# Optimization experiments

Measured on AMD Instinct MI355X. Metric: run time of the kernel, lower is better.

Reference implementation:

```python
import jax, jax.numpy as jnp
import numpy as np

DN = ('NCHW', 'OIHW', 'NCHW')
BLOB_HW = 16  # hard-coded in make_gaussian_blob_maps

_ENC = [(32, 3), (32, 32), (64, 32), (64, 64), (128, 64), (128, 128), (128, 128)]
_DEC = [(64, 128), (64, 64), (32, 64), (32, 32), (16, 32), (16, 16)]


def _conv(x, w, b, stride):
    y = jax.lax.conv_general_dilated(x, w, (stride, stride), 'SAME', dimension_numbers=DN)
    return y + b[None, :, None, None]


def _tconv(x, w, b):
    # decoder stride-2 stage: 'iteratively doubling the input width'
    y = jax.lax.conv_transpose(x, w, (2, 2), 'SAME', dimension_numbers=DN)
    return y + b[None, :, None, None]


def setup_inputs() -> dict:
    key = jax.random.key(0)
    keys = jax.random.split(key, 1 + 2 * (len(_ENC) + len(_DEC)))
    inp = {'x': jax.random.normal(keys[0], (4, 8, 3, 128, 128), jnp.float32)}
    i = 1
    for j, (o, c) in enumerate(_ENC):
        inp[f'enc_w{j}'] = 0.05 * jax.random.normal(keys[i], (o, c, 3, 3), jnp.float32); i += 1
        inp[f'enc_b{j}'] = 0.05 * jax.random.normal(keys[i], (o,), jnp.float32); i += 1
    for j, (o, c) in enumerate(_DEC):
        inp[f'dec_w{j}'] = 0.05 * jax.random.normal(keys[i], (o, c, 3, 3), jnp.float32); i += 1
        inp[f'dec_b{j}'] = 0.05 * jax.random.normal(keys[i], (o,), jnp.float32); i += 1
    return inp


def _forward(x, enc_w0, enc_b0, enc_w1, enc_b1, enc_w2, enc_b2, enc_w3, enc_b3,
             enc_w4, enc_b4, enc_w5, enc_b5, enc_w6, enc_b6,
             dec_w0, dec_b0, dec_w1, dec_b1, dec_w2, dec_b2,
             dec_w3, dec_b3, dec_w4, dec_b4, dec_w5, dec_b5):
    N, T = x.shape[0], x.shape[1]
    xi = x.reshape((N * T,) + x.shape[2:])  # (B, 3, 128, 128)
    # ---- encoder ----
    h = _conv(xi, enc_w0, enc_b0, 1)                              # Identity act
    h = _conv(h, enc_w1, enc_b1, 1)                               # Identity act
    h = jax.nn.leaky_relu(_conv(h, enc_w2, enc_b2, 2), 0.2)       # 128 -> 64
    h = jax.nn.leaky_relu(_conv(h, enc_w3, enc_b3, 1), 0.2)
    h = jax.nn.leaky_relu(_conv(h, enc_w4, enc_b4, 2), 0.2)       # 64 -> 32
    h = jax.nn.leaky_relu(_conv(h, enc_w5, enc_b5, 1), 0.2)
    R = jax.nn.softplus(_conv(h, enc_w6, enc_b6, 2))              # (B, K, 16, 16)
    B, K, H, W = R.shape
    # ---- keypoint presence: mean over spatial dims ----
    mu = R.sum((2, 3)) / (H * W)                                  # (B, K)
    # ---- normalize_feature_maps: faithful net effect of the in-place loop,
    # which ends up dividing each batch item by the ORIGINAL sum of its LAST map ----
    denom = R[:, K - 1].sum((1, 2))                               # (B,)
    D = R / denom[:, None, None, None]
    # ---- average_feature_maps: spatial-index weighted sum (soft-argmax) ----
    gh = jnp.arange(H, dtype=R.dtype)
    gw = jnp.arange(W, dtype=R.dtype)
    c0 = jnp.einsum('bkhw,h->bk', D, gh)                          # row coord
    c1 = jnp.einsum('bkhw,w->bk', D, gw)                          # col coord
    # ---- gaussian blob maps: mu * exp(-0.5 * ||(u,v) - c||^2), sigma = 1 ----
    u = jnp.arange(BLOB_HW, dtype=R.dtype)[:, None]               # (16, 1)
    v = jnp.arange(BLOB_HW, dtype=R.dtype)[None, :]               # (1, 16)
    d2 = (u[None, None] - c0[:, :, None, None]) ** 2 + (v[None, None] - c1[:, :, None, None]) ** 2
    maps = mu[:, :, None, None] * jnp.exp(-0.5 * d2)              # (B, K, 16, 16)
    # ---- decoder ----
    g = jax.nn.relu(_tconv(maps, dec_w0, dec_b0))                 # 16 -> 32
    g = jax.nn.relu(_conv(g, dec_w1, dec_b1, 1))
    g = jax.nn.relu(_tconv(g, dec_w2, dec_b2))                    # 32 -> 64
    g = jax.nn.relu(_conv(g, dec_w3, dec_b3, 1))
    g = jax.nn.relu(_tconv(g, dec_w4, dec_b4))                    # 64 -> 128
    g = jax.nn.relu(_conv(g, dec_w5, dec_b5, 1))
    return g  # original forward returns the un-reshaped (N*T, C, H, W) tensor


def reference(x, enc_w0, enc_b0, enc_w1, enc_b1, enc_w2, enc_b2, enc_w3, enc_b3,
              enc_w4, enc_b4, enc_w5, enc_b5, enc_w6, enc_b6,
              dec_w0, dec_b0, dec_w1, dec_b1, dec_w2, dec_b2,
              dec_w3, dec_b3, dec_w4, dec_b4, dec_w5, dec_b5):
    return _forward(x, enc_w0, enc_b0, enc_w1, enc_b1, enc_w2, enc_b2, enc_w3, enc_b3,
                    enc_w4, enc_b4, enc_w5, enc_b5, enc_w6, enc_b6,
                    dec_w0, dec_b0, dec_w1, dec_b1, dec_w2, dec_b2,
                    dec_w3, dec_b3, dec_w4, dec_b4, dec_w5, dec_b5)
```

## Files before the change

kernel.cpp:

```cpp
#include <hip/hip_runtime.h>
#include <math.h>


enum { ACT_ID = 0, ACT_LRELU = 1, ACT_SOFTPLUS = 2, ACT_RELU = 3 };

template<int ACT>
__device__ __forceinline__ float act_fn(float x) {
  if (ACT == ACT_LRELU)    return x >= 0.f ? x : 0.2f * x;
  if (ACT == ACT_SOFTPLUS) return fmaxf(x, 0.f) + log1pf(expf(-fabsf(x)));
  if (ACT == ACT_RELU)     return fmaxf(x, 0.f);
  return x;
}

template<int ACT, int NC, int CPT>
__global__ __launch_bounds__(256)
void conv_s1(const float* __restrict__ in, const float* __restrict__ w,
             const float* __restrict__ bias, float* __restrict__ out,
             int Cin, int Cout, int H, int W) {
  const int cogs = Cout / NC;
  const int gx  = blockIdx.x;
  const int cog = gx % cogs;
  const int b   = gx / cogs;
  const int co0 = cog * NC;
  const int Wq  = W / CPT;
  const int items = H * Wq;
  const int item  = blockIdx.y * 256 + threadIdx.x;
  if (item >= items) return;
  const int y  = item / Wq;
  const int x0 = (item - y * Wq) * CPT;

  const int HW = H * W;
  const float* ib = in + (size_t)b * Cin * HW;

  const bool okT = (y > 0), okB = (y < H - 1);
  const bool okL = (x0 > 0), okR = (x0 + CPT < W);
  const int ym = okT ? (y - 1) : 0;
  const int yp = okB ? (y + 1) : 0;
  const int xl = okL ? (x0 - 1) : 0;
  const int xr = okR ? (x0 + CPT) : 0;

  float acc[NC][CPT];
  #pragma unroll
  for (int u = 0; u < NC; ++u)
    #pragma unroll
    for (int q = 0; q < CPT; ++q) acc[u][q] = 0.f;

  for (int ci = 0; ci < Cin; ++ci) {
    const float* p = ib + ci * HW;
    const float* wci = w + ((size_t)co0 * Cin + ci) * 9;
    #pragma unroll
    for (int dy = 0; dy < 3; ++dy) {
      const int  ry    = (dy == 0) ? ym : ((dy == 1) ? y : yp);
      const bool okRow = (dy == 0) ? okT : ((dy == 1) ? true : okB);
      const float* r = p + ry * W;
      float v[CPT + 2];
      if (CPT == 4) {
        float  lf = r[xl];
        float4 m  = *(const float4*)(r + x0);
        float  rf = r[xr];
        v[0] = (okRow && okL) ? lf : 0.f;
        v[1] = okRow ? m.x : 0.f;
        v[2] = okRow ? m.y : 0.f;
        v[3] = okRow ? m.z : 0.f;
        v[4] = okRow ? m.w : 0.f;
        v[5] = (okRow && okR) ? rf : 0.f;
      } else {
        v[0] = (okRow && okL) ? r[xl] : 0.f;
        #pragma unroll
        for (int q = 0; q < CPT; ++q) v[1 + q] = okRow ? r[x0 + q] : 0.f;
        v[CPT + 1] = (okRow && okR) ? r[xr] : 0.f;
      }
      #pragma unroll
      for (int u = 0; u < NC; ++u) {
        const float* wp = wci + (size_t)u * Cin * 9 + dy * 3;
        const float w0 = wp[0], w1 = wp[1], w2 = wp[2];
        #pragma unroll
        for (int q = 0; q < CPT; ++q)
          acc[u][q] += v[q] * w0 + v[q + 1] * w1 + v[q + 2] * w2;
      }
    }
  }

  #pragma unroll
  for (int u = 0; u < NC; ++u) {
    const float bv = bias[co0 + u];
    float* op = out + ((size_t)(b * Cout + co0 + u) * H + y) * W + x0;
    if (CPT == 4) {
      float4 r4;
      r4.x = act_fn<ACT>(acc[u][0] + bv);
      r4.y = act_fn<ACT>(acc[u][1] + bv);
      r4.z = act_fn<ACT>(acc[u][2] + bv);
      r4.w = act_fn<ACT>(acc[u][3] + bv);
      *(float4*)op = r4;
    } else {
      #pragma unroll
      for (int q = 0; q < CPT; ++q) op[q] = act_fn<ACT>(acc[u][q] + bv);
    }
  }
}

template<int ACT, int NC, int CPT>
__global__ __launch_bounds__(256)
void conv_s2(const float* __restrict__ in, const float* __restrict__ w,
             const float* __restrict__ bias, float* __restrict__ out,
             int Cin, int Cout, int H, int W) {
  const int Ho = H >> 1, Wo = W >> 1;
  const int cogs = Cout / NC;
  const int gx  = blockIdx.x;
  const int cog = gx % cogs;
  const int b   = gx / cogs;
  const int co0 = cog * NC;
  const int Wq  = Wo / CPT;
  const int items = Ho * Wq;
  const int item  = blockIdx.y * 256 + threadIdx.x;
  if (item >= items) return;
  const int y  = item / Wq;
  const int x0 = (item - y * Wq) * CPT;
  const int ix = 2 * x0;

  const int HW = H * W;
  const float* ib = in + (size_t)b * Cin * HW;

  const int iy0 = 2 * y, iy1 = 2 * y + 1, iy2 = 2 * y + 2;
  const bool okB = (iy2 < H);
  const int iy2c = okB ? iy2 : 0;
  const bool okR = (ix + 2 * CPT < W);
  const int ixr  = okR ? (ix + 2 * CPT) : 0;

  float acc[NC][CPT];
  #pragma unroll
  for (int u = 0; u < NC; ++u)
    #pragma unroll
    for (int q = 0; q < CPT; ++q) acc[u][q] = 0.f;

  for (int ci = 0; ci < Cin; ++ci) {
    const float* p = ib + ci * HW;
    const float* wci = w + ((size_t)co0 * Cin + ci) * 9;
    #pragma unroll
    for (int dy = 0; dy < 3; ++dy) {
      const int  ry    = (dy == 0) ? iy0 : ((dy == 1) ? iy1 : iy2c);
      const bool okRow = (dy < 2) || okB;
      const float* r = p + ry * W;
      float v[2 * CPT + 1];
      if (CPT == 4) {
        float4 m0 = *(const float4*)(r + ix);
        float4 m1 = *(const float4*)(r + ix + 4);
        float  rf = r[ixr];
        v[0] = okRow ? m0.x : 0.f; v[1] = okRow ? m0.y : 0.f;
        v[2] = okRow ? m0.z : 0.f; v[3] = okRow ? m0.w : 0.f;
        v[4] = okRow ? m1.x : 0.f; v[5] = okRow ? m1.y : 0.f;
        v[6] = okRow ? m1.z : 0.f; v[7] = okRow ? m1.w : 0.f;
        v[8] = (okRow && okR) ? rf : 0.f;
      } else {
        #pragma unroll
        for (int q = 0; q < 2 * CPT; ++q) v[q] = okRow ? r[ix + q] : 0.f;
        v[2 * CPT] = (okRow && okR) ? r[ixr] : 0.f;
      }
      #pragma unroll
      for (int u = 0; u < NC; ++u) {
        const float* wp = wci + (size_t)u * Cin * 9 + dy * 3;
        const float w0 = wp[0], w1 = wp[1], w2 = wp[2];
        #pragma unroll
        for (int q = 0; q < CPT; ++q)
          acc[u][q] += v[2*q] * w0 + v[2*q + 1] * w1 + v[2*q + 2] * w2;
      }
    }
  }

  #pragma unroll
  for (int u = 0; u < NC; ++u) {
    const float bv = bias[co0 + u];
    float* op = out + ((size_t)(b * Cout + co0 + u) * Ho + y) * Wo + x0;
    if (CPT == 4) {
      float4 r4;
      r4.x = act_fn<ACT>(acc[u][0] + bv);
      r4.y = act_fn<ACT>(acc[u][1] + bv);
      r4.z = act_fn<ACT>(acc[u][2] + bv);
      r4.w = act_fn<ACT>(acc[u][3] + bv);
      *(float4*)op = r4;
    } else {
      #pragma unroll
      for (int q = 0; q < CPT; ++q) op[q] = act_fn<ACT>(acc[u][q] + bv);
    }
  }
}

template<int ACT, int NC>
__global__ __launch_bounds__(256)
void tconv(const float* __restrict__ in, const float* __restrict__ w,
           const float* __restrict__ bias, float* __restrict__ out,
           int Cin, int Cout, int Hin) {
  const int cogs = Cout / NC;
  const int gx  = blockIdx.x;
  const int cog = gx % cogs;
  const int b   = gx / cogs;
  const int co0 = cog * NC;
  const int items = Hin * Hin;
  const int item  = blockIdx.y * 256 + threadIdx.x;
  if (item >= items) return;
  const int i = item / Hin;
  const int j = item - i * Hin;

  const float* ib = in + (size_t)b * Cin * items;
  const bool okT = (i > 0), okL = (j > 0);
  const int im = okT ? i - 1 : 0;
  const int jm = okL ? j - 1 : 0;

  float a00[NC], a01[NC], a10[NC], a11[NC];
  #pragma unroll
  for (int u = 0; u < NC; ++u) { a00[u]=0.f; a01[u]=0.f; a10[u]=0.f; a11[u]=0.f; }

  for (int ci = 0; ci < Cin; ++ci) {
    const float* p = ib + ci * items;
    float xtl = p[im*Hin + jm]; xtl = (okT && okL) ? xtl : 0.f;
    float xtr = p[im*Hin + j];  xtr = okT ? xtr : 0.f;
    float xbl = p[i*Hin + jm];  xbl = okL ? xbl : 0.f;
    float xbr = p[i*Hin + j];
    const float* wci = w + ((size_t)co0 * Cin + ci) * 9;
    #pragma unroll
    for (int u = 0; u < NC; ++u) {
      const float* wp = wci + (size_t)u * Cin * 9;
      const float w00 = wp[0], w01 = wp[1], w02 = wp[2];
      const float w10 = wp[3], w11 = wp[4], w12 = wp[5];
      const float w20 = wp[6], w21 = wp[7], w22 = wp[8];
      a00[u] += xtl*w00 + xtr*w02 + xbl*w20 + xbr*w22;
      a01[u] += xtr*w01 + xbr*w21;
      a10[u] += xbl*w10 + xbr*w12;
      a11[u] += xbr*w11;
    }
  }

  const int Ho = Hin * 2;
  #pragma unroll
  for (int u = 0; u < NC; ++u) {
    const float bv = bias[co0 + u];
    float* op = out + (size_t)(b * Cout + co0 + u) * Ho * Ho + (2*i) * Ho + 2*j;
    float2 t0, t1;
    t0.x = act_fn<ACT>(a00[u] + bv); t0.y = act_fn<ACT>(a01[u] + bv);
    t1.x = act_fn<ACT>(a10[u] + bv); t1.y = act_fn<ACT>(a11[u] + bv);
    *(float2*)op = t0;
    *(float2*)(op + Ho) = t1;
  }
}

__global__ __launch_bounds__(64)
void kp_reduce(const float* __restrict__ R, float* __restrict__ S,
               float* __restrict__ Sh, float* __restrict__ Sw) {
  const int bk = blockIdx.x;
  const int t = threadIdx.x;
  const float* p = R + (size_t)bk * 256;
  float s = 0.f, sh = 0.f, sw = 0.f;
  #pragma unroll
  for (int q = 0; q < 4; ++q) {
    int idx = t + q * 64;
    float v = p[idx];
    s  += v;
    sh += v * (float)(idx >> 4);
    sw += v * (float)(idx & 15);
  }
  #pragma unroll
  for (int off = 32; off > 0; off >>= 1) {
    s  += __shfl_down(s, off);
    sh += __shfl_down(sh, off);
    sw += __shfl_down(sw, off);
  }
  if (t == 0) { S[bk] = s; Sh[bk] = sh; Sw[bk] = sw; }
}

__global__ __launch_bounds__(256)
void kp_maps(const float* __restrict__ S, const float* __restrict__ Sh,
             const float* __restrict__ Sw, float* __restrict__ maps, int K) {
  const int bk = blockIdx.x;
  const int b = bk / K;
  const int t = threadIdx.x;
  const float s   = S[bk];
  const float den = S[b * K + (K - 1)];
  const float mu  = s * (1.0f / 256.0f);
  const float c0  = Sh[bk] / den;
  const float c1  = Sw[bk] / den;
  const float u = (float)(t >> 4);
  const float v = (float)(t & 15);
  const float d2 = (u - c0) * (u - c0) + (v - c1) * (v - c1);
  maps[(size_t)bk * 256 + t] = mu * expf(-0.5f * d2);
}

extern "C" void kernel_launch(void* const* d_in, const int* in_sizes, int n_in,
                              void* d_out, int out_size, void* d_ws, size_t ws_size,
                              hipStream_t stream) {
  const int B = 32;
  const float* x = (const float*)d_in[0];
  const float* ew[7]; const float* eb[7];
  for (int j = 0; j < 7; ++j) { ew[j] = (const float*)d_in[1 + 2*j]; eb[j] = (const float*)d_in[2 + 2*j]; }
  const float* dw[6]; const float* db[6];
  for (int j = 0; j < 6; ++j) { dw[j] = (const float*)d_in[15 + 2*j]; db[j] = (const float*)d_in[16 + 2*j]; }

  float* ws   = (float*)d_ws;
  float* bufA = ws;
  float* bufB = bufA + 16777216;
  float* R    = bufB + 16777216;
  float* maps = R + 1048576;
  float* S    = maps + 1048576;
  float* Sh   = S + 4096;
  float* Sw   = Sh + 4096;
  float* outp = (float*)d_out;

  dim3 blk(256);

  conv_s1<ACT_ID,      8,4><<<dim3(B*4,  16), blk, 0, stream>>>(x,    ew[0], eb[0], bufA, 3,   32,  128, 128);
  conv_s1<ACT_ID,      8,4><<<dim3(B*4,  16), blk, 0, stream>>>(bufA, ew[1], eb[1], bufB, 32,  32,  128, 128);
  conv_s2<ACT_LRELU,   8,4><<<dim3(B*8,   4), blk, 0, stream>>>(bufB, ew[2], eb[2], bufA, 32,  64,  128, 128);
  conv_s1<ACT_LRELU,   8,4><<<dim3(B*8,   4), blk, 0, stream>>>(bufA, ew[3], eb[3], bufB, 64,  64,  64,  64);
  conv_s2<ACT_LRELU,   8,4><<<dim3(B*16,  1), blk, 0, stream>>>(bufB, ew[4], eb[4], bufA, 64,  128, 64,  64);
  conv_s1<ACT_LRELU,   8,4><<<dim3(B*16,  1), blk, 0, stream>>>(bufA, ew[5], eb[5], bufB, 128, 128, 32,  32);
  conv_s2<ACT_SOFTPLUS,8,1><<<dim3(B*16,  1), blk, 0, stream>>>(bufB, ew[6], eb[6], R,    128, 128, 32,  32);

  kp_reduce<<<dim3(B*128), dim3(64), 0, stream>>>(R, S, Sh, Sw);
  kp_maps  <<<dim3(B*128), blk, 0, stream>>>(S, Sh, Sw, maps, 128);

  tconv<ACT_RELU,   8>  <<<dim3(B*8,   1), blk, 0, stream>>>(maps, dw[0], db[0], bufA, 128, 64, 16);
  conv_s1<ACT_RELU, 8,4><<<dim3(B*8,   1), blk, 0, stream>>>(bufA, dw[1], db[1], bufB, 64,  64, 32, 32);
  tconv<ACT_RELU,   8>  <<<dim3(B*4,   4), blk, 0, stream>>>(bufB, dw[2], db[2], bufA, 64,  32, 32);
  conv_s1<ACT_RELU, 8,4><<<dim3(B*4,   4), blk, 0, stream>>>(bufA, dw[3], db[3], bufB, 32,  32, 64, 64);
  tconv<ACT_RELU,   8>  <<<dim3(B*2,  16), blk, 0, stream>>>(bufB, dw[4], db[4], bufA, 32,  16, 64);
  conv_s1<ACT_RELU, 8,4><<<dim3(B*2,  16), blk, 0, stream>>>(bufA, dw[5], db[5], outp, 16,  16, 128, 128);
}
```

Measured before the change: 1.375 ms.

## Split-K over input channels for small-spatial convs, double-buffer loads, retune tiles

Adds a split-K template parameter so the low-resolution convolutions divide input channels across two grid slices, writing partial sums that a new combine kernel adds together with bias and activation applied. This raises the block count for layers that previously launched only a few blocks per image. It also software-pipelines the per-channel loads (double-buffered registers) in the conv and tconv kernels, and lowers columns-per-thread or channels-per-block for several layers to expose more threads. In exchange it adds extra partial-sum global traffic and extra kernel launches.

New measurement: 1.320 ms. 4.0% less time.

```diff
diff --git a/kernel.cpp b/kernel.cpp
--- a/kernel.cpp
+++ b/kernel.cpp
@@ -12,11 +12,11 @@
   return x;
 }
 
-template<int ACT, int NC, int CPT>
+template<int ACT, int NC, int CPT, int KS>
 __global__ __launch_bounds__(256)
 void conv_s1(const float* __restrict__ in, const float* __restrict__ w,
              const float* __restrict__ bias, float* __restrict__ out,
-             int Cin, int Cout, int H, int W) {
+             int Cin, int Cout, int H, int W, size_t kstride) {
   const int cogs = Cout / NC;
   const int gx  = blockIdx.x;
   const int cog = gx % cogs;
@@ -31,6 +31,10 @@
 
   const int HW = H * W;
   const float* ib = in + (size_t)b * Cin * HW;
+  const int nci = Cin / KS;
+  const int ci0 = (KS > 1) ? (int)blockIdx.z * nci : 0;
+  const int ci1 = ci0 + nci;
+  float* outbase = out + ((KS > 1) ? (size_t)blockIdx.z * kstride : 0);
 
   const bool okT = (y > 0), okB = (y < H - 1);
   const bool okL = (x0 > 0), okR = (x0 + CPT < W);
@@ -41,69 +45,109 @@
 
   float acc[NC][CPT];
   #pragma unroll
-  for (int u = 0; u < NC; ++u)
+  for (int u = 0; u < NC; ++u) {
     #pragma unroll
     for (int q = 0; q < CPT; ++q) acc[u][q] = 0.f;
-
-  for (int ci = 0; ci < Cin; ++ci) {
+  }
+
+  constexpr int RV = CPT + 2;
+
+  auto load_rows = [&](float* v, int ci) {
     const float* p = ib + ci * HW;
-    const float* wci = w + ((size_t)co0 * Cin + ci) * 9;
     #pragma unroll
     for (int dy = 0; dy < 3; ++dy) {
-      const int  ry    = (dy == 0) ? ym : ((dy == 1) ? y : yp);
+      const int ry = (dy == 0) ? ym : ((dy == 1) ? y : yp);
+      const float* r = p + ry * W;
+      float* o = v + dy * RV;
+      o[0] = r[xl];
+      if constexpr (CPT == 4) {
+        float4 m = *(const float4*)(r + x0);
+        o[1] = m.x; o[2] = m.y; o[3] = m.z; o[4] = m.w;
+      } else if constexpr (CPT == 2) {
+        float2 m = *(const float2*)(r + x0);
+        o[1] = m.x; o[2] = m.y;
+      } else {
+        #pragma unroll
+        for (int q = 0; q < CPT; ++q) o[1 + q] = r[x0 + q];
+      }
+      o[CPT + 1] = r[xr];
+    }
+  };
+
+  auto fma_rows = [&](float* v, int ci) {
+    #pragma unroll
+    for (int dy = 0; dy < 3; ++dy) {
       const bool okRow = (dy == 0) ? okT : ((dy == 1) ? true : okB);
-      const float* r = p + ry * W;
-      float v[CPT + 2];
-      if (CPT == 4) {
-        float  lf = r[xl];
-        float4 m  = *(const float4*)(r + x0);
-        float  rf = r[xr];
-        v[0] = (okRow && okL) ? lf : 0.f;
-        v[1] = okRow ? m.x : 0.f;
-        v[2] = okRow ? m.y : 0.f;
-        v[3] = okRow ? m.z : 0.f;
-        v[4] = okRow ? m.w : 0.f;
-        v[5] = (okRow && okR) ? rf : 0.f;
-      } else {
-        v[0] = (okRow && okL) ? r[xl] : 0.f;
-        #pragma unroll
-        for (int q = 0; q < CPT; ++q) v[1 + q] = okRow ? r[x0 + q] : 0.f;
-        v[CPT + 1] = (okRow && okR) ? r[xr] : 0.f;
-      }
+      float* o = v + dy * RV;
+      o[0] = (okRow && okL) ? o[0] : 0.f;
       #pragma unroll
-      for (int u = 0; u < NC; ++u) {
-        const float* wp = wci + (size_t)u * Cin * 9 + dy * 3;
-        const float w0 = wp[0], w1 = wp[1], w2 = wp[2];
+      for (int q = 1; q <= CPT; ++q) o[q] = okRow ? o[q] : 0.f;
+      o[CPT + 1] = (okRow && okR) ? o[CPT + 1] : 0.f;
+    }
+    #pragma unroll
+    for (int u = 0; u < NC; ++u) {
+      const float* wp = w + ((size_t)(co0 + u) * Cin + ci) * 9;
+      #pragma unroll
+      for (int dy = 0; dy < 3; ++dy) {
+        const float w0 = wp[dy*3], w1 = wp[dy*3+1], w2 = wp[dy*3+2];
+        const float* o = v + dy * RV;
         #pragma unroll
         for (int q = 0; q < CPT; ++q)
-          acc[u][q] += v[q] * w0 + v[q + 1] * w1 + v[q + 2] * w2;
-      }
-    }
+          acc[u][q] += o[q] * w0 + o[q + 1] * w1 + o[q + 2] * w2;
+      }
+    }
+  };
+
+  float va[3 * RV], vb[3 * RV];
+  load_rows(va, ci0);
+  int ci = ci0;
+  while (true) {
+    if (ci + 1 < ci1) load_rows(vb, ci + 1);
+    fma_rows(va, ci);
+    ++ci; if (ci >= ci1) break;
+    if (ci + 1 < ci1) load_rows(va, ci + 1);
+    fma_rows(vb, ci);
+    ++ci; if (ci >= ci1) break;
   }
 
   #pragma unroll
   for (int u = 0; u < NC; ++u) {
-    const float bv = bias[co0 + u];
-    float* op = out + ((size_t)(b * Cout + co0 + u) * H + y) * W + x0;
-    if (CPT == 4) {
-      float4 r4;
-      r4.x = act_fn<ACT>(acc[u][0] + bv);
-      r4.y = act_fn<ACT>(acc[u][1] + bv);
-      r4.z = act_fn<ACT>(acc[u][2] + bv);
-      r4.w = act_fn<ACT>(acc[u][3] + bv);
-      *(float4*)op = r4;
+    float* op = outbase + ((size_t)(b * Cout + co0 + u) * H + y) * W + x0;
+    if constexpr (KS > 1) {
+      if constexpr (CPT == 4) {
+        float4 r4 = {acc[u][0], acc[u][1], acc[u][2], acc[u][3]};
+        *(float4*)op = r4;
+      } else if constexpr (CPT == 2) {
+        float2 r2 = {acc[u][0], acc[u][1]};
+        *(float2*)op = r2;
+      } else {
+        #pragma unroll
+        for (int q = 0; q < CPT; ++q) op[q] = acc[u][q];
+      }
     } else {
-      #pragma unroll
-      for (int q = 0; q < CPT; ++q) op[q] = act_fn<ACT>(acc[u][q] + bv);
-    }
-  }
-}
-
-template<int ACT, int NC, int CPT>
+      const float bv = bias[co0 + u];
+      if constexpr (CPT == 4) {
+        float4 r4;
+        r4.x = act_fn<ACT>(acc[u][0] + bv); r4.y = act_fn<ACT>(acc[u][1] + bv);
+        r4.z = act_fn<ACT>(acc[u][2] + bv); r4.w = act_fn<ACT>(acc[u][3] + bv);
+        *(float4*)op = r4;
+      } else if constexpr (CPT == 2) {
+        float2 r2;
+        r2.x = act_fn<ACT>(acc[u][0] + bv); r2.y = act_fn<ACT>(acc[u][1] + bv);
+        *(float2*)op = r2;
+      } else {
+        #pragma unroll
+        for (int q = 0; q < CPT; ++q) op[q] = act_fn<ACT>(acc[u][q] + bv);
+      }
+    }
+  }
+}
+
+template<int ACT, int NC, int CPT, int KS>
 __global__ __launch_bounds__(256)
 void conv_s2(const float* __restrict__ in, const float* __restrict__ w,
              const float* __restrict__ bias, float* __restrict__ out,
-             int Cin, int Cout, int H, int W) {
+             int Cin, int Cout, int H, int W, size_t kstride) {
   const int Ho = H >> 1, Wo = W >> 1;
   const int cogs = Cout / NC;
   const int gx  = blockIdx.x;
@@ -120,6 +164,10 @@
 
   const int HW = H * W;
   const float* ib = in + (size_t)b * Cin * HW;
+  const int nci = Cin / KS;
+  const int ci0 = (KS > 1) ? (int)blockIdx.z * nci : 0;
+  const int ci1 = ci0 + nci;
+  float* outbase = out + ((KS > 1) ? (size_t)blockIdx.z * kstride : 0);
 
   const int iy0 = 2 * y, iy1 = 2 * y + 1, iy2 = 2 * y + 2;
   const bool okB = (iy2 < H);
@@ -129,58 +177,100 @@
 
   float acc[NC][CPT];
   #pragma unroll
-  for (int u = 0; u < NC; ++u)
+  for (int u = 0; u < NC; ++u) {
     #pragma unroll
     for (int q = 0; q < CPT; ++q) acc[u][q] = 0.f;
-
-  for (int ci = 0; ci < Cin; ++ci) {
+  }
+
+  constexpr int RV = 2 * CPT + 1;
+
+  auto load_rows = [&](float* v, int ci) {
     const float* p = ib + ci * HW;
-    const float* wci = w + ((size_t)co0 * Cin + ci) * 9;
     #pragma unroll
     for (int dy = 0; dy < 3; ++dy) {
-      const int  ry    = (dy == 0) ? iy0 : ((dy == 1) ? iy1 : iy2c);
-      const bool okRow = (dy < 2) || okB;
+      const int ry = (dy == 0) ? iy0 : ((dy == 1) ? iy1 : iy2c);
       const float* r = p + ry * W;
-      float v[2 * CPT + 1];
-      if (CPT == 4) {
+      float* o = v + dy * RV;
+      if constexpr (CPT == 4) {
         float4 m0 = *(const float4*)(r + ix);
         float4 m1 = *(const float4*)(r + ix + 4);
-        float  rf = r[ixr];
-        v[0] = okRow ? m0.x : 0.f; v[1] = okRow ? m0.y : 0.f;
-        v[2] = okRow ? m0.z : 0.f; v[3] = okRow ? m0.w : 0.f;
-        v[4] = okRow ? m1.x : 0.f; v[5] = okRow ? m1.y : 0.f;
-        v[6] = okRow ? m1.z : 0.f; v[7] = okRow ? m1.w : 0.f;
-        v[8] = (okRow && okR) ? rf : 0.f;
-      } else {
-        #pragma unroll
-        for (int q = 0; q < 2 * CPT; ++q) v[q] = okRow ? r[ix + q] : 0.f;
-        v[2 * CPT] = (okRow && okR) ? r[ixr] : 0.f;
-      }
+        o[0]=m0.x; o[1]=m0.y; o[2]=m0.z; o[3]=m0.w;
+        o[4]=m1.x; o[5]=m1.y; o[6]=m1.z; o[7]=m1.w;
+      } else if constexpr (CPT == 2) {
+        float4 m0 = *(const float4*)(r + ix);
+        o[0]=m0.x; o[1]=m0.y; o[2]=m0.z; o[3]=m0.w;
+      } else {
+        float2 m0 = *(const float2*)(r + ix);
+        o[0]=m0.x; o[1]=m0.y;
+      }
+      o[2*CPT] = r[ixr];
+    }
+  };
+
+  auto fma_rows = [&](float* v, int ci) {
+    #pragma unroll
+    for (int dy = 0; dy < 3; ++dy) {
+      const bool okRow = (dy < 2) || okB;
+      float* o = v + dy * RV;
       #pragma unroll
-      for (int u = 0; u < NC; ++u) {
-        const float* wp = wci + (size_t)u * Cin * 9 + dy * 3;
-        const float w0 = wp[0], w1 = wp[1], w2 = wp[2];
+      for (int q = 0; q < 2 * CPT; ++q) o[q] = okRow ? o[q] : 0.f;
+      o[2*CPT] = (okRow && okR) ? o[2*CPT] : 0.f;
+    }
+    #pragma unroll
+    for (int u = 0; u < NC; ++u) {
+      const float* wp = w + ((size_t)(co0 + u) * Cin + ci) * 9;
+      #pragma unroll
+      for (int dy = 0; dy < 3; ++dy) {
+        const float w0 = wp[dy*3], w1 = wp[dy*3+1], w2 = wp[dy*3+2];
+        const float* o = v + dy * RV;
         #pragma unroll
         for (int q = 0; q < CPT; ++q)
-          acc[u][q] += v[2*q] * w0 + v[2*q + 1] * w1 + v[2*q + 2] * w2;
-      }
-    }
+          acc[u][q] += o[2*q] * w0 + o[2*q + 1] * w1 + o[2*q + 2] * w2;
+      }
+    }
+  };
+
+  float va[3 * RV], vb[3 * RV];
+  load_rows(va, ci0);
+  int ci = ci0;
+  while (true) {
+    if (ci + 1 < ci1) load_rows(vb, ci + 1);
+    fma_rows(va, ci);
+    ++ci; if (ci >= ci1) break;
+    if (ci + 1 < ci1) load_rows(va, ci + 1);
+    fma_rows(vb, ci);
+    ++ci; if (ci >= ci1) break;
   }
 
   #pragma unroll
   for (int u = 0; u < NC; ++u) {
-    const float bv = bias[co0 + u];
-    float* op = out + ((size_t)(b * Cout + co0 + u) * Ho + y) * Wo + x0;
-    if (CPT == 4) {
-      float4 r4;
-      r4.x = act_fn<ACT>(acc[u][0] + bv);
-      r4.y = act_fn<ACT>(acc[u][1] + bv);
-      r4.z = act_fn<ACT>(acc[u][2] + bv);
-      r4.w = act_fn<ACT>(acc[u][3] + bv);
-      *(float4*)op = r4;
+    float* op = outbase + ((size_t)(b * Cout + co0 + u) * Ho + y) * Wo + x0;
+    if constexpr (KS > 1) {
+      if constexpr (CPT == 4) {
+        float4 r4 = {acc[u][0], acc[u][1], acc[u][2], acc[u][3]};
+        *(float4*)op = r4;
+      } else if constexpr (CPT == 2) {
+        float2 r2 = {acc[u][0], acc[u][1]};
+        *(float2*)op = r2;
+      } else {
+        #pragma unroll
+        for (int q = 0; q < CPT; ++q) op[q] = acc[u][q];
+      }
     } else {
-      #pragma unroll
-      for (int q = 0; q < CPT; ++q) op[q] = act_fn<ACT>(acc[u][q] + bv);
+      const float bv = bias[co0 + u];
+      if constexpr (CPT == 4) {
+        float4 r4;
+        r4.x = act_fn<ACT>(acc[u][0] + bv); r4.y = act_fn<ACT>(acc[u][1] + bv);
+        r4.z = act_fn<ACT>(acc[u][2] + bv); r4.w = act_fn<ACT>(acc[u][3] + bv);
+        *(float4*)op = r4;
+      } else if constexpr (CPT == 2) {
+        float2 r2;
+        r2.x = act_fn<ACT>(acc[u][0] + bv); r2.y = act_fn<ACT>(acc[u][1] + bv);
+        *(float2*)op = r2;
+      } else {
+        #pragma unroll
+        for (int q = 0; q < CPT; ++q) op[q] = act_fn<ACT>(acc[u][q] + bv);
+      }
     }
   }
 }
@@ -210,16 +300,21 @@
   #pragma unroll
   for (int u = 0; u < NC; ++u) { a00[u]=0.f; a01[u]=0.f; a10[u]=0.f; a11[u]=0.f; }
 
-  for (int ci = 0; ci < Cin; ++ci) {
+  auto load4 = [&](float* v, int ci) {
     const float* p = ib + ci * items;
-    float xtl = p[im*Hin + jm]; xtl = (okT && okL) ? xtl : 0.f;
-    float xtr = p[im*Hin + j];  xtr = okT ? xtr : 0.f;
-    float xbl = p[i*Hin + jm];  xbl = okL ? xbl : 0.f;
-    float xbr = p[i*Hin + j];
-    const float* wci = w + ((size_t)co0 * Cin + ci) * 9;
+    v[0] = p[im*Hin + jm];
+    v[1] = p[im*Hin + j];
+    v[2] = p[i*Hin + jm];
+    v[3] = p[i*Hin + j];
+  };
+  auto fma4 = [&](float* v, int ci) {
+    float xtl = (okT && okL) ? v[0] : 0.f;
+    float xtr = okT ? v[1] : 0.f;
+    float xbl = okL ? v[2] : 0.f;
+    float xbr = v[3];
     #pragma unroll
     for (int u = 0; u < NC; ++u) {
-      const float* wp = wci + (size_t)u * Cin * 9;
+      const float* wp = w + ((size_t)(co0 + u) * Cin + ci) * 9;
       const float w00 = wp[0], w01 = wp[1], w02 = wp[2];
       const float w10 = wp[3], w11 = wp[4], w12 = wp[5];
       const float w20 = wp[6], w21 = wp[7], w22 = wp[8];
@@ -228,6 +323,18 @@
       a10[u] += xbl*w10 + xbr*w12;
       a11[u] += xbr*w11;
     }
+  };
+
+  float va[4], vb[4];
+  load4(va, 0);
+  int ci = 0;
+  while (true) {
+    if (ci + 1 < Cin) load4(vb, ci + 1);
+    fma4(va, ci);
+    ++ci; if (ci >= Cin) break;
+    if (ci + 1 < Cin) load4(va, ci + 1);
+    fma4(vb, ci);
+    ++ci; if (ci >= Cin) break;
   }
 
   const int Ho = Hin * 2;
@@ -241,6 +348,26 @@
     *(float2*)op = t0;
     *(float2*)(op + Ho) = t1;
   }
+}
+
+template<int ACT>
+__global__ __launch_bounds__(256)
+void combine2(const float* __restrict__ P0, const float* __restrict__ P1,
+              const float* __restrict__ bias, float* __restrict__ out,
+              int C, int HW, int n4) {
+  const int i = blockIdx.x * 256 + threadIdx.x;
+  if (i >= n4) return;
+  const int e = i * 4;
+  const int c = (e / HW) % C;
+  float4 a = ((const float4*)P0)[i];
+  float4 b = ((const float4*)P1)[i];
+  const float bv = bias[c];
+  float4 r;
+  r.x = act_fn<ACT>(a.x + b.x + bv);
+  r.y = act_fn<ACT>(a.y + b.y + bv);
+  r.z = act_fn<ACT>(a.z + b.z + bv);
+  r.w = act_fn<ACT>(a.w + b.w + bv);
+  ((float4*)out)[i] = r;
 }
 
 __global__ __launch_bounds__(64)
@@ -306,21 +433,31 @@
 
   dim3 blk(256);
 
-  conv_s1<ACT_ID,      8,4><<<dim3(B*4,  16), blk, 0, stream>>>(x,    ew[0], eb[0], bufA, 3,   32,  128, 128);
-  conv_s1<ACT_ID,      8,4><<<dim3(B*4,  16), blk, 0, stream>>>(bufA, ew[1], eb[1], bufB, 32,  32,  128, 128);
-  conv_s2<ACT_LRELU,   8,4><<<dim3(B*8,   4), blk, 0, stream>>>(bufB, ew[2], eb[2], bufA, 32,  64,  128, 128);
-  conv_s1<ACT_LRELU,   8,4><<<dim3(B*8,   4), blk, 0, stream>>>(bufA, ew[3], eb[3], bufB, 64,  64,  64,  64);
-  conv_s2<ACT_LRELU,   8,4><<<dim3(B*16,  1), blk, 0, stream>>>(bufB, ew[4], eb[4], bufA, 64,  128, 64,  64);
-  conv_s1<ACT_LRELU,   8,4><<<dim3(B*16,  1), blk, 0, stream>>>(bufA, ew[5], eb[5], bufB, 128, 128, 32,  32);
-  conv_s2<ACT_SOFTPLUS,8,1><<<dim3(B*16,  1), blk, 0, stream>>>(bufB, ew[6], eb[6], R,    128, 128, 32,  32);
+  conv_s1<ACT_ID,   8,4,1><<<dim3(B*4, 16),    blk, 0, stream>>>(x,    ew[0], eb[0], bufA, 3,   32,  128, 128, 0);
+  conv_s1<ACT_ID,   8,4,1><<<dim3(B*4, 16),    blk, 0, stream>>>(bufA, ew[1], eb[1], bufB, 32,  32,  128, 128, 0);
+  conv_s2<ACT_LRELU,8,4,1><<<dim3(B*8,  4),    blk, 0, stream>>>(bufB, ew[2], eb[2], bufA, 32,  64,  128, 128, 0);
+  conv_s1<ACT_LRELU,8,4,1><<<dim3(B*8,  4),    blk, 0, stream>>>(bufA, ew[3], eb[3], bufB, 64,  64,  64,  64,  0);
+  conv_s2<ACT_LRELU,8,2,1><<<dim3(B*16, 2),    blk, 0, stream>>>(bufB, ew[4], eb[4], bufA, 64,  128, 64,  64,  0);
+
+  float* P5 = bufA + 8388608;
+  conv_s1<ACT_LRELU,8,4,2><<<dim3(B*16, 1, 2), blk, 0, stream>>>(bufA, ew[5], eb[5], P5, 128, 128, 32, 32, 4194304);
+  combine2<ACT_LRELU><<<dim3(4096), blk, 0, stream>>>(P5, P5 + 4194304, eb[5], bufB, 128, 1024, 1048576);
+
+  float* P6 = bufA;
+  conv_s2<ACT_SOFTPLUS,8,1,2><<<dim3(B*16, 1, 2), blk, 0, stream>>>(bufB, ew[6], eb[6], P6, 128, 128, 32, 32, 1048576);
+  combine2<ACT_SOFTPLUS><<<dim3(1024), blk, 0, stream>>>(P6, P6 + 1048576, eb[6], R, 128, 256, 262144);
 
   kp_reduce<<<dim3(B*128), dim3(64), 0, stream>>>(R, S, Sh, Sw);
   kp_maps  <<<dim3(B*128), blk, 0, stream>>>(S, Sh, Sw, maps, 128);
 
-  tconv<ACT_RELU,   8>  <<<dim3(B*8,   1), blk, 0, stream>>>(maps, dw[0], db[0], bufA, 128, 64, 16);
-  conv_s1<ACT_RELU, 8,4><<<dim3(B*8,   1), blk, 0, stream>>>(bufA, dw[1], db[1], bufB, 64,  64, 32, 32);
-  tconv<ACT_RELU,   8>  <<<dim3(B*4,   4), blk, 0, stream>>>(bufB, dw[2], db[2], bufA, 64,  32, 32);
-  conv_s1<ACT_RELU, 8,4><<<dim3(B*4,   4), blk, 0, stream>>>(bufA, dw[3], db[3], bufB, 32,  32, 64, 64);
-  tconv<ACT_RELU,   8>  <<<dim3(B*2,  16), blk, 0, stream>>>(bufB, dw[4], db[4], bufA, 32,  16, 64);
-  conv_s1<ACT_RELU, 8,4><<<dim3(B*2,  16), blk, 0, stream>>>(bufA, dw[5], db[5], outp, 16,  16, 128, 128);
-}
+  tconv<ACT_RELU,2><<<dim3(B*32, 1), blk, 0, stream>>>(maps, dw[0], db[0], bufA, 128, 64, 16);
+
+  float* PD1 = bufA + 4194304;
+  conv_s1<ACT_RELU,8,2,2><<<dim3(B*8, 2, 2), blk, 0, stream>>>(bufA, dw[1], db[1], PD1, 64, 64, 32, 32, 2097152);
+  combine2<ACT_RELU><<<dim3(2048), blk, 0, stream>>>(PD1, PD1 + 2097152, db[1], bufB, 64, 1024, 524288);
+
+  tconv<ACT_RELU,4>      <<<dim3(B*8,  4), blk, 0, stream>>>(bufB, dw[2], db[2], bufA, 64, 32, 32);
+  conv_s1<ACT_RELU,8,2,1><<<dim3(B*4,  8), blk, 0, stream>>>(bufA, dw[3], db[3], bufB, 32, 32, 64, 64, 0);
+  tconv<ACT_RELU,8>      <<<dim3(B*2, 16), blk, 0, stream>>>(bufB, dw[4], db[4], bufA, 32, 16, 64);
+  conv_s1<ACT_RELU,8,4,1><<<dim3(B*2, 16), blk, 0, stream>>>(bufA, dw[5], db[5], outp, 16, 16, 128, 128, 0);
+}
```

## Specialize conv kernels on compile-time shapes, add interior fast path, retune grids

Applied to the files above, without the earlier changes.

Turns channel counts and spatial sizes into template parameters so index math and loop bounds become compile-time constants. Adds a boundary-free interior path that loads the halo without predication, with a masked path for edge threads. Retunes NC/CPT per layer to launch more blocks on the small late layers, which were badly under-occupied. The bounds check on item was removed, so the grids must now exactly cover the work items.

Measured after the change: 1.522 ms. 1.11x slower.

```diff
diff --git a/kernel.cpp b/kernel.cpp
--- a/kernel.cpp
+++ b/kernel.cpp
@@ -12,229 +12,296 @@
   return x;
 }
 
-template<int ACT, int NC, int CPT>
+template<int ACT, int NC, int CPT, int CIN, int COUT, int HH, int WW>
 __global__ __launch_bounds__(256)
 void conv_s1(const float* __restrict__ in, const float* __restrict__ w,
-             const float* __restrict__ bias, float* __restrict__ out,
-             int Cin, int Cout, int H, int W) {
-  const int cogs = Cout / NC;
+             const float* __restrict__ bias, float* __restrict__ out) {
+  constexpr int cogs = COUT / NC;
+  constexpr int HW = HH * WW;
+  constexpr int Wq = WW / CPT;
   const int gx  = blockIdx.x;
   const int cog = gx % cogs;
   const int b   = gx / cogs;
   const int co0 = cog * NC;
-  const int Wq  = W / CPT;
-  const int items = H * Wq;
-  const int item  = blockIdx.y * 256 + threadIdx.x;
-  if (item >= items) return;
+  const int item = blockIdx.y * 256 + threadIdx.x;
   const int y  = item / Wq;
   const int x0 = (item - y * Wq) * CPT;
-
-  const int HW = H * W;
-  const float* ib = in + (size_t)b * Cin * HW;
-
-  const bool okT = (y > 0), okB = (y < H - 1);
-  const bool okL = (x0 > 0), okR = (x0 + CPT < W);
-  const int ym = okT ? (y - 1) : 0;
-  const int yp = okB ? (y + 1) : 0;
-  const int xl = okL ? (x0 - 1) : 0;
-  const int xr = okR ? (x0 + CPT) : 0;
+  const float* bp = in + (size_t)b * CIN * HW + y * WW + x0;
 
   float acc[NC][CPT];
-  #pragma unroll
-  for (int u = 0; u < NC; ++u)
-    #pragma unroll
+#pragma unroll
+  for (int u = 0; u < NC; ++u) {
+#pragma unroll
     for (int q = 0; q < CPT; ++q) acc[u][q] = 0.f;
-
-  for (int ci = 0; ci < Cin; ++ci) {
-    const float* p = ib + ci * HW;
-    const float* wci = w + ((size_t)co0 * Cin + ci) * 9;
-    #pragma unroll
-    for (int dy = 0; dy < 3; ++dy) {
-      const int  ry    = (dy == 0) ? ym : ((dy == 1) ? y : yp);
-      const bool okRow = (dy == 0) ? okT : ((dy == 1) ? true : okB);
-      const float* r = p + ry * W;
-      float v[CPT + 2];
-      if (CPT == 4) {
-        float  lf = r[xl];
-        float4 m  = *(const float4*)(r + x0);
-        float  rf = r[xr];
-        v[0] = (okRow && okL) ? lf : 0.f;
-        v[1] = okRow ? m.x : 0.f;
-        v[2] = okRow ? m.y : 0.f;
-        v[3] = okRow ? m.z : 0.f;
-        v[4] = okRow ? m.w : 0.f;
-        v[5] = (okRow && okR) ? rf : 0.f;
-      } else {
-        v[0] = (okRow && okL) ? r[xl] : 0.f;
-        #pragma unroll
-        for (int q = 0; q < CPT; ++q) v[1 + q] = okRow ? r[x0 + q] : 0.f;
-        v[CPT + 1] = (okRow && okR) ? r[xr] : 0.f;
-      }
-      #pragma unroll
-      for (int u = 0; u < NC; ++u) {
-        const float* wp = wci + (size_t)u * Cin * 9 + dy * 3;
-        const float w0 = wp[0], w1 = wp[1], w2 = wp[2];
-        #pragma unroll
-        for (int q = 0; q < CPT; ++q)
-          acc[u][q] += v[q] * w0 + v[q + 1] * w1 + v[q + 2] * w2;
-      }
-    }
-  }
-
-  #pragma unroll
+  }
+
+  float v[3][CPT + 2];
+
+  auto fma_all = [&](int ci) {
+#pragma unroll
+    for (int u = 0; u < NC; ++u) {
+      const float* q = w + ((size_t)(co0 + u) * CIN + ci) * 9;
+#pragma unroll
+      for (int dy = 0; dy < 3; ++dy) {
+        const float w0 = q[dy * 3], w1 = q[dy * 3 + 1], w2 = q[dy * 3 + 2];
+#pragma unroll
+        for (int t = 0; t < CPT; ++t) {
+          acc[u][t] = fmaf(v[dy][t],     w0, acc[u][t]);
+          acc[u][t] = fmaf(v[dy][t + 1], w1, acc[u][t]);
+          acc[u][t] = fmaf(v[dy][t + 2], w2, acc[u][t]);
+        }
+      }
+    }
+  };
+
+  const bool okT = (y > 0), okB = (y < HH - 1);
+  const bool okL = (x0 > 0), okR = (x0 + CPT < WW);
+
+  if (okT && okB && okL && okR) {
+    for (int ci = 0; ci < CIN; ++ci) {
+      const float* p = bp + (size_t)ci * HW;
+#pragma unroll
+      for (int dy = 0; dy < 3; ++dy) {
+        const float* r = p + (dy - 1) * WW;
+        v[dy][0] = r[-1];
+        if constexpr (CPT == 4) {
+          float4 m = *(const float4*)r;
+          v[dy][1] = m.x; v[dy][2] = m.y; v[dy][3] = m.z; v[dy][4] = m.w;
+        } else if constexpr (CPT == 2) {
+          float2 m = *(const float2*)r;
+          v[dy][1] = m.x; v[dy][2] = m.y;
+        } else {
+          v[dy][1] = r[0];
+        }
+        v[dy][CPT + 1] = r[CPT];
+      }
+      fma_all(ci);
+    }
+  } else {
+    const int ro0 = okT ? -WW : 0;
+    const int ro2 = okB ?  WW : 0;
+    const int xlo = okL ? -1 : 0;
+    const int xro = okR ? CPT : 0;
+    for (int ci = 0; ci < CIN; ++ci) {
+      const float* p = bp + (size_t)ci * HW;
+#pragma unroll
+      for (int dy = 0; dy < 3; ++dy) {
+        const int  ro    = (dy == 0) ? ro0 : ((dy == 1) ? 0 : ro2);
+        const bool okRow = (dy == 0) ? okT : ((dy == 1) ? true : okB);
+        const float* r = p + ro;
+        float lf = r[xlo];
+        v[dy][0] = (okRow && okL) ? lf : 0.f;
+#pragma unroll
+        for (int t = 0; t < CPT; ++t) {
+          float mv = r[t];
+          v[dy][1 + t] = okRow ? mv : 0.f;
+        }
+        float rf = r[xro];
+        v[dy][CPT + 1] = (okRow && okR) ? rf : 0.f;
+      }
+      fma_all(ci);
+    }
+  }
+
+#pragma unroll
   for (int u = 0; u < NC; ++u) {
     const float bv = bias[co0 + u];
-    float* op = out + ((size_t)(b * Cout + co0 + u) * H + y) * W + x0;
-    if (CPT == 4) {
+    float* op = out + ((size_t)(b * COUT + co0 + u) * HH + y) * WW + x0;
+    if constexpr (CPT == 4) {
       float4 r4;
-      r4.x = act_fn<ACT>(acc[u][0] + bv);
-      r4.y = act_fn<ACT>(acc[u][1] + bv);
-      r4.z = act_fn<ACT>(acc[u][2] + bv);
-      r4.w = act_fn<ACT>(acc[u][3] + bv);
+      r4.x = act_fn<ACT>(acc[u][0] + bv); r4.y = act_fn<ACT>(acc[u][1] + bv);
+      r4.z = act_fn<ACT>(acc[u][2] + bv); r4.w = act_fn<ACT>(acc[u][3] + bv);
       *(float4*)op = r4;
+    } else if constexpr (CPT == 2) {
+      float2 r2;
+      r2.x = act_fn<ACT>(acc[u][0] + bv); r2.y = act_fn<ACT>(acc[u][1] + bv);
+      *(float2*)op = r2;
     } else {
-      #pragma unroll
-      for (int q = 0; q < CPT; ++q) op[q] = act_fn<ACT>(acc[u][q] + bv);
-    }
-  }
-}
-
-template<int ACT, int NC, int CPT>
+      op[0] = act_fn<ACT>(acc[u][0] + bv);
+    }
+  }
+}
+
+template<int ACT, int NC, int CPT, int CIN, int COUT, int HH, int WW>
 __global__ __launch_bounds__(256)
 void conv_s2(const float* __restrict__ in, const float* __restrict__ w,
-             const float* __restrict__ bias, float* __restrict__ out,
-             int Cin, int Cout, int H, int W) {
-  const int Ho = H >> 1, Wo = W >> 1;
-  const int cogs = Cout / NC;
+             const float* __restrict__ bias, float* __restrict__ out) {
+  constexpr int Ho = HH / 2, Wo = WW / 2;
+  constexpr int cogs = COUT / NC;
+  constexpr int HW = HH * WW;
+  constexpr int Wq = Wo / CPT;
   const int gx  = blockIdx.x;
   const int cog = gx % cogs;
   const int b   = gx / cogs;
   const int co0 = cog * NC;
-  const int Wq  = Wo / CPT;
-  const int items = Ho * Wq;
-  const int item  = blockIdx.y * 256 + threadIdx.x;
-  if (item >= items) return;
+  const int item = blockIdx.y * 256 + threadIdx.x;
   const int y  = item / Wq;
   const int x0 = (item - y * Wq) * CPT;
   const int ix = 2 * x0;
-
-  const int HW = H * W;
-  const float* ib = in + (size_t)b * Cin * HW;
-
-  const int iy0 = 2 * y, iy1 = 2 * y + 1, iy2 = 2 * y + 2;
-  const bool okB = (iy2 < H);
-  const int iy2c = okB ? iy2 : 0;
-  const bool okR = (ix + 2 * CPT < W);
-  const int ixr  = okR ? (ix + 2 * CPT) : 0;
+  const float* bp = in + (size_t)b * CIN * HW + (2 * y) * WW + ix;
 
   float acc[NC][CPT];
-  #pragma unroll
-  for (int u = 0; u < NC; ++u)
-    #pragma unroll
+#pragma unroll
+  for (int u = 0; u < NC; ++u) {
+#pragma unroll
     for (int q = 0; q < CPT; ++q) acc[u][q] = 0.f;
-
-  for (int ci = 0; ci < Cin; ++ci) {
-    const float* p = ib + ci * HW;
-    const float* wci = w + ((size_t)co0 * Cin + ci) * 9;
-    #pragma unroll
-    for (int dy = 0; dy < 3; ++dy) {
-      const int  ry    = (dy == 0) ? iy0 : ((dy == 1) ? iy1 : iy2c);
-      const bool okRow = (dy < 2) || okB;
-      const float* r = p + ry * W;
-      float v[2 * CPT + 1];
-      if (CPT == 4) {
-        float4 m0 = *(const float4*)(r + ix);
-        float4 m1 = *(const float4*)(r + ix + 4);
-        float  rf = r[ixr];
-        v[0] = okRow ? m0.x : 0.f; v[1] = okRow ? m0.y : 0.f;
-        v[2] = okRow ? m0.z : 0.f; v[3] = okRow ? m0.w : 0.f;
-        v[4] = okRow ? m1.x : 0.f; v[5] = okRow ? m1.y : 0.f;
-        v[6] = okRow ? m1.z : 0.f; v[7] = okRow ? m1.w : 0.f;
-        v[8] = (okRow && okR) ? rf : 0.f;
-      } else {
-        #pragma unroll
-        for (int q = 0; q < 2 * CPT; ++q) v[q] = okRow ? r[ix + q] : 0.f;
-        v[2 * CPT] = (okRow && okR) ? r[ixr] : 0.f;
-      }
-      #pragma unroll
-      for (int u = 0; u < NC; ++u) {
-        const float* wp = wci + (size_t)u * Cin * 9 + dy * 3;
-        const float w0 = wp[0], w1 = wp[1], w2 = wp[2];
-        #pragma unroll
-        for (int q = 0; q < CPT; ++q)
-          acc[u][q] += v[2*q] * w0 + v[2*q + 1] * w1 + v[2*q + 2] * w2;
-      }
-    }
-  }
-
-  #pragma unroll
+  }
+
+  float v[3][2 * CPT + 1];
+
+  auto fma_all = [&](int ci) {
+#pragma unroll
+    for (int u = 0; u < NC; ++u) {
+      const float* q = w + ((size_t)(co0 + u) * CIN + ci) * 9;
+#pragma unroll
+      for (int dy = 0; dy < 3; ++dy) {
+        const float w0 = q[dy * 3], w1 = q[dy * 3 + 1], w2 = q[dy * 3 + 2];
+#pragma unroll
+        for (int t = 0; t < CPT; ++t) {
+          acc[u][t] = fmaf(v[dy][2 * t],     w0, acc[u][t]);
+          acc[u][t] = fmaf(v[dy][2 * t + 1], w1, acc[u][t]);
+          acc[u][t] = fmaf(v[dy][2 * t + 2], w2, acc[u][t]);
+        }
+      }
+    }
+  };
+
+  const bool okB = (2 * y + 2 < HH);
+  const bool okR = (ix + 2 * CPT < WW);
+
+  if (okB && okR) {
+    for (int ci = 0; ci < CIN; ++ci) {
+      const float* p = bp + (size_t)ci * HW;
+#pragma unroll
+      for (int dy = 0; dy < 3; ++dy) {
+        const float* r = p + dy * WW;
+        if constexpr (CPT == 4) {
+          float4 m0 = *(const float4*)r;
+          float4 m1 = *(const float4*)(r + 4);
+          v[dy][0]=m0.x; v[dy][1]=m0.y; v[dy][2]=m0.z; v[dy][3]=m0.w;
+          v[dy][4]=m1.x; v[dy][5]=m1.y; v[dy][6]=m1.z; v[dy][7]=m1.w;
+        } else if constexpr (CPT == 2) {
+          float4 m0 = *(const float4*)r;
+          v[dy][0]=m0.x; v[dy][1]=m0.y; v[dy][2]=m0.z; v[dy][3]=m0.w;
+        } else {
+          float2 m0 = *(const float2*)r;
+          v[dy][0]=m0.x; v[dy][1]=m0.y;
+        }
+        v[dy][2 * CPT] = r[2 * CPT];
+      }
+      fma_all(ci);
+    }
+  } else {
+    const int ro2 = okB ? 2 * WW : 0;
+    const int xro = okR ? 2 * CPT : 0;
+    for (int ci = 0; ci < CIN; ++ci) {
+      const float* p = bp + (size_t)ci * HW;
+#pragma unroll
+      for (int dy = 0; dy < 3; ++dy) {
+        const int  ro    = (dy == 2) ? ro2 : dy * WW;
+        const bool okRow = (dy < 2) || okB;
+        const float* r = p + ro;
+        if constexpr (CPT == 4) {
+          float4 m0 = *(const float4*)r;
+          float4 m1 = *(const float4*)(r + 4);
+          v[dy][0]=m0.x; v[dy][1]=m0.y; v[dy][2]=m0.z; v[dy][3]=m0.w;
+          v[dy][4]=m1.x; v[dy][5]=m1.y; v[dy][6]=m1.z; v[dy][7]=m1.w;
+        } else if constexpr (CPT == 2) {
+          float4 m0 = *(const float4*)r;
+          v[dy][0]=m0.x; v[dy][1]=m0.y; v[dy][2]=m0.z; v[dy][3]=m0.w;
+        } else {
+          float2 m0 = *(const float2*)r;
+          v[dy][0]=m0.x; v[dy][1]=m0.y;
+        }
+        if (!okRow) {
+#pragma unroll
+          for (int t = 0; t < 2 * CPT; ++t) v[dy][t] = 0.f;
+        }
+        float rf = r[xro];
+        v[dy][2 * CPT] = (okRow && okR) ? rf : 0.f;
+      }
+      fma_all(ci);
+    }
+  }
+
+#pragma unroll
   for (int u = 0; u < NC; ++u) {
     const float bv = bias[co0 + u];
-    float* op = out + ((size_t)(b * Cout + co0 + u) * Ho + y) * Wo + x0;
-    if (CPT == 4) {
+    float* op = out + ((size_t)(b * COUT + co0 + u) * Ho + y) * Wo + x0;
+    if constexpr (CPT == 4) {
       float4 r4;
-      r4.x = act_fn<ACT>(acc[u][0] + bv);
-      r4.y = act_fn<ACT>(acc[u][1] + bv);
-      r4.z = act_fn<ACT>(acc[u][2] + bv);
-      r4.w = act_fn<ACT>(acc[u][3] + bv);
+      r4.x = act_fn<ACT>(acc[u][0] + bv); r4.y = act_fn<ACT>(acc[u][1] + bv);
+      r4.z = act_fn<ACT>(acc[u][2] + bv); r4.w = act_fn<ACT>(acc[u][3] + bv);
       *(float4*)op = r4;
+    } else if constexpr (CPT == 2) {
+      float2 r2;
+      r2.x = act_fn<ACT>(acc[u][0] + bv); r2.y = act_fn<ACT>(acc[u][1] + bv);
+      *(float2*)op = r2;
     } else {
-      #pragma unroll
-      for (int q = 0; q < CPT; ++q) op[q] = act_fn<ACT>(acc[u][q] + bv);
-    }
-  }
-}
-
-template<int ACT, int NC>
+      op[0] = act_fn<ACT>(acc[u][0] + bv);
+    }
+  }
+}
+
+template<int ACT, int NC, int CIN, int COUT, int HIN>
 __global__ __launch_bounds__(256)
 void tconv(const float* __restrict__ in, const float* __restrict__ w,
-           const float* __restrict__ bias, float* __restrict__ out,
-           int Cin, int Cout, int Hin) {
-  const int cogs = Cout / NC;
+           const float* __restrict__ bias, float* __restrict__ out) {
+  constexpr int cogs = COUT / NC;
+  constexpr int items = HIN * HIN;
   const int gx  = blockIdx.x;
   const int cog = gx % cogs;
   const int b   = gx / cogs;
   const int co0 = cog * NC;
-  const int items = Hin * Hin;
-  const int item  = blockIdx.y * 256 + threadIdx.x;
-  if (item >= items) return;
-  const int i = item / Hin;
-  const int j = item - i * Hin;
-
-  const float* ib = in + (size_t)b * Cin * items;
-  const bool okT = (i > 0), okL = (j > 0);
-  const int im = okT ? i - 1 : 0;
-  const int jm = okL ? j - 1 : 0;
+  const int item = blockIdx.y * 256 + threadIdx.x;
+  const int i = item / HIN;
+  const int j = item - i * HIN;
+  const float* bp = in + (size_t)b * CIN * items + i * HIN + j;
 
   float a00[NC], a01[NC], a10[NC], a11[NC];
-  #pragma unroll
+#pragma unroll
   for (int u = 0; u < NC; ++u) { a00[u]=0.f; a01[u]=0.f; a10[u]=0.f; a11[u]=0.f; }
 
-  for (int ci = 0; ci < Cin; ++ci) {
-    const float* p = ib + ci * items;
-    float xtl = p[im*Hin + jm]; xtl = (okT && okL) ? xtl : 0.f;
-    float xtr = p[im*Hin + j];  xtr = okT ? xtr : 0.f;
-    float xbl = p[i*Hin + jm];  xbl = okL ? xbl : 0.f;
-    float xbr = p[i*Hin + j];
-    const float* wci = w + ((size_t)co0 * Cin + ci) * 9;
-    #pragma unroll
+  auto fmab = [&](float xtl, float xtr, float xbl, float xbr, int ci) {
+#pragma unroll
     for (int u = 0; u < NC; ++u) {
-      const float* wp = wci + (size_t)u * Cin * 9;
-      const float w00 = wp[0], w01 = wp[1], w02 = wp[2];
-      const float w10 = wp[3], w11 = wp[4], w12 = wp[5];
-      const float w20 = wp[6], w21 = wp[7], w22 = wp[8];
-      a00[u] += xtl*w00 + xtr*w02 + xbl*w20 + xbr*w22;
-      a01[u] += xtr*w01 + xbr*w21;
-      a10[u] += xbl*w10 + xbr*w12;
-      a11[u] += xbr*w11;
-    }
-  }
-
-  const int Ho = Hin * 2;
-  #pragma unroll
+      const float* q = w + ((size_t)(co0 + u) * CIN + ci) * 9;
+      a00[u] = fmaf(xtl, q[0], a00[u]);
+      a00[u] = fmaf(xtr, q[2], a00[u]);
+      a00[u] = fmaf(xbl, q[6], a00[u]);
+      a00[u] = fmaf(xbr, q[8], a00[u]);
+      a01[u] = fmaf(xtr, q[1], a01[u]);
+      a01[u] = fmaf(xbr, q[7], a01[u]);
+      a10[u] = fmaf(xbl, q[3], a10[u]);
+      a10[u] = fmaf(xbr, q[5], a10[u]);
+      a11[u] = fmaf(xbr, q[4], a11[u]);
+    }
+  };
+
+  if (i > 0 && j > 0) {
+    for (int ci = 0; ci < CIN; ++ci) {
+      const float* p = bp + (size_t)ci * items;
+      fmab(p[-HIN - 1], p[-HIN], p[-1], p[0], ci);
+    }
+  } else {
+    const bool okT = (i > 0), okL = (j > 0);
+    const int to = okT ? -HIN : 0;
+    const int lo = okL ? -1 : 0;
+    for (int ci = 0; ci < CIN; ++ci) {
+      const float* p = bp + (size_t)ci * items;
+      float xtl = p[to + lo]; xtl = (okT && okL) ? xtl : 0.f;
+      float xtr = p[to];      xtr = okT ? xtr : 0.f;
+      float xbl = p[lo];      xbl = okL ? xbl : 0.f;
+      float xbr = p[0];
+      fmab(xtl, xtr, xbl, xbr, ci);
+    }
+  }
+
+  constexpr int Ho = HIN * 2;
+#pragma unroll
   for (int u = 0; u < NC; ++u) {
     const float bv = bias[co0 + u];
-    float* op = out + (size_t)(b * Cout + co0 + u) * Ho * Ho + (2*i) * Ho + 2*j;
+    float* op = out + (size_t)(b * COUT + co0 + u) * Ho * Ho + (2 * i) * Ho + 2 * j;
     float2 t0, t1;
     t0.x = act_fn<ACT>(a00[u] + bv); t0.y = act_fn<ACT>(a01[u] + bv);
     t1.x = act_fn<ACT>(a10[u] + bv); t1.y = act_fn<ACT>(a11[u] + bv);
@@ -250,7 +317,7 @@
   const int t = threadIdx.x;
   const float* p = R + (size_t)bk * 256;
   float s = 0.f, sh = 0.f, sw = 0.f;
-  #pragma unroll
+#pragma unroll
   for (int q = 0; q < 4; ++q) {
     int idx = t + q * 64;
     float v = p[idx];
@@ -258,7 +325,7 @@
     sh += v * (float)(idx >> 4);
     sw += v * (float)(idx & 15);
   }
-  #pragma unroll
+#pragma unroll
   for (int off = 32; off > 0; off >>= 1) {
     s  += __shfl_down(s, off);
     sh += __shfl_down(sh, off);
@@ -306,21 +373,21 @@
 
   dim3 blk(256);
 
-  conv_s1<ACT_ID,      8,4><<<dim3(B*4,  16), blk, 0, stream>>>(x,    ew[0], eb[0], bufA, 3,   32,  128, 128);
-  conv_s1<ACT_ID,      8,4><<<dim3(B*4,  16), blk, 0, stream>>>(bufA, ew[1], eb[1], bufB, 32,  32,  128, 128);
-  conv_s2<ACT_LRELU,   8,4><<<dim3(B*8,   4), blk, 0, stream>>>(bufB, ew[2], eb[2], bufA, 32,  64,  128, 128);
-  conv_s1<ACT_LRELU,   8,4><<<dim3(B*8,   4), blk, 0, stream>>>(bufA, ew[3], eb[3], bufB, 64,  64,  64,  64);
-  conv_s2<ACT_LRELU,   8,4><<<dim3(B*16,  1), blk, 0, stream>>>(bufB, ew[4], eb[4], bufA, 64,  128, 64,  64);
-  conv_s1<ACT_LRELU,   8,4><<<dim3(B*16,  1), blk, 0, stream>>>(bufA, ew[5], eb[5], bufB, 128, 128, 32,  32);
-  conv_s2<ACT_SOFTPLUS,8,1><<<dim3(B*16,  1), blk, 0, stream>>>(bufB, ew[6], eb[6], R,    128, 128, 32,  32);
+  conv_s1<ACT_ID,      8,4,  3, 32,128,128><<<dim3(B*4, 16), blk, 0, stream>>>(x,    ew[0], eb[0], bufA);
+  conv_s1<ACT_ID,      8,4, 32, 32,128,128><<<dim3(B*4, 16), blk, 0, stream>>>(bufA, ew[1], eb[1], bufB);
+  conv_s2<ACT_LRELU,   8,4, 32, 64,128,128><<<dim3(B*8,  4), blk, 0, stream>>>(bufB, ew[2], eb[2], bufA);
+  conv_s1<ACT_LRELU,   8,4, 64, 64, 64, 64><<<dim3(B*8,  4), blk, 0, stream>>>(bufA, ew[3], eb[3], bufB);
+  conv_s2<ACT_LRELU,   8,2, 64,128, 64, 64><<<dim3(B*16, 2), blk, 0, stream>>>(bufB, ew[4], eb[4], bufA);
+  conv_s1<ACT_LRELU,   8,2,128,128, 32, 32><<<dim3(B*16, 2), blk, 0, stream>>>(bufA, ew[5], eb[5], bufB);
+  conv_s2<ACT_SOFTPLUS,4,1,128,128, 32, 32><<<dim3(B*32, 1), blk, 0, stream>>>(bufB, ew[6], eb[6], R);
 
   kp_reduce<<<dim3(B*128), dim3(64), 0, stream>>>(R, S, Sh, Sw);
   kp_maps  <<<dim3(B*128), blk, 0, stream>>>(S, Sh, Sw, maps, 128);
 
-  tconv<ACT_RELU,   8>  <<<dim3(B*8,   1), blk, 0, stream>>>(maps, dw[0], db[0], bufA, 128, 64, 16);
-  conv_s1<ACT_RELU, 8,4><<<dim3(B*8,   1), blk, 0, stream>>>(bufA, dw[1], db[1], bufB, 64,  64, 32, 32);
-  tconv<ACT_RELU,   8>  <<<dim3(B*4,   4), blk, 0, stream>>>(bufB, dw[2], db[2], bufA, 64,  32, 32);
-  conv_s1<ACT_RELU, 8,4><<<dim3(B*4,   4), blk, 0, stream>>>(bufA, dw[3], db[3], bufB, 32,  32, 64, 64);
-  tconv<ACT_RELU,   8>  <<<dim3(B*2,  16), blk, 0, stream>>>(bufB, dw[4], db[4], bufA, 32,  16, 64);
-  conv_s1<ACT_RELU, 8,4><<<dim3(B*2,  16), blk, 0, stream>>>(bufA, dw[5], db[5], outp, 16,  16, 128, 128);
-}
+  tconv<ACT_RELU,2,128, 64,16><<<dim3(B*32, 1), blk, 0, stream>>>(maps, dw[0], db[0], bufA);
+  conv_s1<ACT_RELU,4,2, 64, 64, 32, 32><<<dim3(B*16, 2), blk, 0, stream>>>(bufA, dw[1], db[1], bufB);
+  tconv<ACT_RELU,4, 64, 32,32><<<dim3(B*8,  4), blk, 0, stream>>>(bufB, dw[2], db[2], bufA);
+  conv_s1<ACT_RELU,8,2, 32, 32, 64, 64><<<dim3(B*4,  8), blk, 0, stream>>>(bufA, dw[3], db[3], bufB);
+  tconv<ACT_RELU,8, 32, 16,64><<<dim3(B*2, 16), blk, 0, stream>>>(bufB, dw[4], db[4], bufA);
+  conv_s1<ACT_RELU,8,4, 16, 16,128,128><<<dim3(B*2, 16), blk, 0, stream>>>(bufA, dw[5], db[5], outp);
+}
```
